# Performance work log

Measured on AMD Instinct MI355X. Metric: run time of the kernel, lower is better.

## Reference

```python
import jax, jax.numpy as jnp
import numpy as np

EMBED = 1024
HEADS = 16
HEAD_DIM = EMBED // HEADS


def setup_inputs() -> dict:
    key = jax.random.key(0)
    ks = jax.random.split(key, 10)
    s = 1.0 / np.sqrt(EMBED)
    inp = {
        "x": jax.random.normal(ks[0], (4, 2048, EMBED), dtype=jnp.float32),
        "mask": jax.random.randint(ks[1], (4, 2048), 0, 2, dtype=jnp.int32),
        "Wq": jax.random.uniform(ks[2], (EMBED, EMBED), jnp.float32, -s, s),
        "bq": jax.random.uniform(ks[3], (EMBED,), jnp.float32, -s, s),
        "Wk": jax.random.uniform(ks[4], (EMBED, EMBED), jnp.float32, -s, s),
        "bk": jax.random.uniform(ks[5], (EMBED,), jnp.float32, -s, s),
        "Wv": jax.random.uniform(ks[6], (EMBED, EMBED), jnp.float32, -s, s),
        "bv": jax.random.uniform(ks[7], (EMBED,), jnp.float32, -s, s),
        "Wo": jax.random.uniform(ks[8], (EMBED, EMBED), jnp.float32, -s, s),
        "bo": jax.random.uniform(ks[9], (EMBED,), jnp.float32, -s, s),
    }
    return inp


def reference(x, mask, Wq, bq, Wk, bk, Wv, bv, Wo, bo):
    B, S, E = x.shape
    scale = np.sqrt(HEAD_DIM).astype(np.float32)

    def split_heads(t):  # [B,S,E] -> [B,H,S,D]
        return t.reshape(B, S, HEADS, HEAD_DIM).transpose(0, 2, 1, 3)

    Q = split_heads(x @ Wq.T + bq)
    K = split_heads(x @ Wk.T + bk)
    V = split_heads(x @ Wv.T + bv)

    scores = jnp.einsum("bhqd,bhkd->bhqk", Q, K) / scale  # [B,H,S,S]
    # mask [B,S] broadcast over heads and query dim (key-padding mask)
    scores = jnp.where(mask[:, None, None, :] == 0, -jnp.inf, scores)
    weights = jax.nn.softmax(scores, axis=-1)
    out = jnp.einsum("bhqk,bhkd->bhqd", weights, V)  # [B,H,S,D]
    out = out.transpose(0, 2, 1, 3).reshape(B, S, E)
    return out @ Wo.T + bo
```

## Files before the change

kernel.cpp:

```cpp
#include <hip/hip_runtime.h>

#define BATCH 4
#define SEQ   2048
#define EMBED 1024
#define HEADS 16
#define HDIM  64
#define NTOK  (BATCH*SEQ)

typedef __attribute__((ext_vector_type(8)))  short short8;
typedef __attribute__((ext_vector_type(4)))  float f32x4;
typedef __attribute__((ext_vector_type(16))) float f32x16;

static __device__ __forceinline__ unsigned short f2bf(float f) {
    union { float f; unsigned u; } v; v.f = f;
    return (unsigned short)((v.u + 0x7FFFu + ((v.u >> 16) & 1u)) >> 16);
}
static __device__ __forceinline__ unsigned pk2bf(float lo, float hi) {
    union { float f; unsigned u; } a, b; a.f = lo; b.f = hi;
    return __builtin_amdgcn_perm(b.u + 0x8000u, a.u + 0x8000u, 0x07060302u);
}
static __device__ __forceinline__ void gload_lds16(const unsigned short* g, unsigned short* l) {
    __builtin_amdgcn_global_load_lds(
        (__attribute__((address_space(1))) void*)g,
        (__attribute__((address_space(3))) void*)l, 16, 0, 0);
}

__global__ void cast_f32_bf16(const float* __restrict__ in,
                              unsigned short* __restrict__ out, int n)
{
    int i = (blockIdx.x * 256 + threadIdx.x) * 8;
    if (i >= n) return;
    float4 a = *(const float4*)(in + i);
    float4 b = *(const float4*)(in + i + 4);
    union { int4 v; unsigned short u[8]; } pk;
    pk.u[0] = f2bf(a.x); pk.u[1] = f2bf(a.y); pk.u[2] = f2bf(a.z); pk.u[3] = f2bf(a.w);
    pk.u[4] = f2bf(b.x); pk.u[5] = f2bf(b.y); pk.u[6] = f2bf(b.z); pk.u[7] = f2bf(b.w);
    *(int4*)(out + i) = pk.v;
}

__global__ void cast4_f32_bf16(const float* __restrict__ a, const float* __restrict__ b,
                               const float* __restrict__ c, const float* __restrict__ d,
                               unsigned short* __restrict__ out)
{
    const float* srcs[4] = {a, b, c, d};
    const float* src = srcs[blockIdx.y];
    unsigned short* dst = out + (size_t)blockIdx.y * (EMBED * EMBED);
    int i = (blockIdx.x * 256 + threadIdx.x) * 8;
    float4 x = *(const float4*)(src + i);
    float4 y = *(const float4*)(src + i + 4);
    union { int4 v; unsigned short u[8]; } pk;
    pk.u[0] = f2bf(x.x); pk.u[1] = f2bf(x.y); pk.u[2] = f2bf(x.z); pk.u[3] = f2bf(x.w);
    pk.u[4] = f2bf(y.x); pk.u[5] = f2bf(y.y); pk.u[6] = f2bf(y.z); pk.u[7] = f2bf(y.w);
    *(int4*)(dst + i) = pk.v;
}

__device__ __forceinline__ void gemm_mainloop(const unsigned short* __restrict__ W,
                                              const unsigned short* __restrict__ X,
                                              int f0, int t0, f32x4 acc[4][4])
{
    __shared__ unsigned short Ws[128][32];
    __shared__ unsigned short Xs[128][32];

    const int tid  = threadIdx.x;
    const int lane = tid & 63, m = lane & 15, quad = lane >> 4;
    const int wid  = tid >> 6;
    const int wf   = (wid & 1) * 64;
    const int wt   = (wid >> 1) * 64;

    const int r    = tid >> 2, cc = tid & 3, sw = (tid >> 4) & 3;
    const int gcol = (cc ^ sw) << 3;
    const unsigned short* Wp = W + (size_t)(f0 + r) * EMBED + gcol;
    const unsigned short* Xp = X + (size_t)(t0 + r) * EMBED + gcol;
    unsigned short* WsL = &Ws[0][0] + tid * 8;
    unsigned short* XsL = &Xs[0][0] + tid * 8;

    const int qs = (quad ^ ((m >> 2) & 3)) << 3;

    for (int k0 = 0; k0 < EMBED; k0 += 32) {
        __syncthreads();
        gload_lds16(Wp + k0,              WsL);
        gload_lds16(Wp + k0 + 64 * EMBED, WsL + 2048);
        gload_lds16(Xp + k0,              XsL);
        gload_lds16(Xp + k0 + 64 * EMBED, XsL + 2048);
        __syncthreads();

        short8 af[4], bf4[4];
#pragma unroll
        for (int mb = 0; mb < 4; ++mb)
            af[mb] = *(const short8*)&Ws[wf + mb * 16 + m][qs];
#pragma unroll
        for (int nb = 0; nb < 4; ++nb)
            bf4[nb] = *(const short8*)&Xs[wt + nb * 16 + m][qs];
#pragma unroll
        for (int mb = 0; mb < 4; ++mb)
#pragma unroll
            for (int nb = 0; nb < 4; ++nb)
                acc[mb][nb] = __builtin_amdgcn_mfma_f32_16x16x32_bf16(
                    af[mb], bf4[nb], acc[mb][nb], 0, 0, 0);
    }
}

__global__ __launch_bounds__(256, 2)
void gemm_qkv(const unsigned short* __restrict__ Xb,
              const unsigned short* __restrict__ Wall,
              const float* __restrict__ bq, const float* __restrict__ bk,
              const float* __restrict__ bv,
              unsigned short* __restrict__ Qw, unsigned short* __restrict__ Kw,
              unsigned short* __restrict__ VtG)
{
    const int z  = blockIdx.z;
    const int f0 = blockIdx.x * 128, t0 = blockIdx.y * 128;
    f32x4 acc[4][4] = {};
    gemm_mainloop(Wall + (size_t)z * EMBED * EMBED, Xb, f0, t0, acc);

    const int lane = threadIdx.x & 63, m = lane & 15, quad = lane >> 4;
    const int wid  = threadIdx.x >> 6;
    const int wf = (wid & 1) * 64, wt = (wid >> 1) * 64;

    if (z < 2) {
        const float* bias = z ? bk : bq;
        unsigned short* C = z ? Kw : Qw;
#pragma unroll
        for (int mb = 0; mb < 4; ++mb) {
            const int feat = f0 + wf + mb * 16 + quad * 4;
            float4 bv4 = *(const float4*)&bias[feat];
#pragma unroll
            for (int nb = 0; nb < 4; ++nb) {
                const int tok = t0 + wt + nb * 16 + m;
                ushort4 pk;
                pk.x = f2bf(acc[mb][nb][0] + bv4.x);
                pk.y = f2bf(acc[mb][nb][1] + bv4.y);
                pk.z = f2bf(acc[mb][nb][2] + bv4.z);
                pk.w = f2bf(acc[mb][nb][3] + bv4.w);
                *(ushort4*)(C + (size_t)tok * EMBED + feat) = pk;
            }
        }
    } else {
        const int h = (f0 + wf) >> 6;
#pragma unroll
        for (int mb = 0; mb < 4; ++mb) {
            const int feat  = f0 + wf + mb * 16 + quad * 4;
            const int dbase = mb * 16 + quad * 4;
            float4 bv4 = *(const float4*)&bv[feat];
            float bb[4] = {bv4.x, bv4.y, bv4.z, bv4.w};
#pragma unroll
            for (int nb = 0; nb < 4; ++nb) {
                const int tok = t0 + wt + nb * 16 + m;
                const int b   = tok >> 11;
                const int s   = tok & (SEQ - 1);
#pragma unroll
                for (int r = 0; r < 4; ++r) {
                    VtG[((size_t)(b * HEADS + h) * HDIM + dbase + r) * SEQ + s] =
                        f2bf(acc[mb][nb][r] + bb[r]);
                }
            }
        }
    }
}

__global__ __launch_bounds__(256, 4)
void attn_mfma(const unsigned short* __restrict__ Qb,
               const unsigned short* __restrict__ Kb,
               const unsigned short* __restrict__ VtG,
               const int* __restrict__ mask,
               unsigned short* __restrict__ Ob)
{
    __shared__ unsigned short Ks[64][72];
    __shared__ unsigned short Vs[64][72];

    const int tid  = threadIdx.x;
    const int bid  = blockIdx.x;
    const int qb   = bid & 15;
    const int h    = (bid >> 4) & 15;
    const int b    = bid >> 8;
    const int wid  = tid >> 6, lane = tid & 63;
    const int q32  = lane & 31, hi = lane >> 5;
    const int tb   = b * SEQ;
    const int q    = qb * 128 + wid * 32 + q32;

    const unsigned short* qrow = Qb + (size_t)(tb + q) * EMBED + h * HDIM;
    short8 qf[4];
#pragma unroll
    for (int st = 0; st < 4; ++st)
        qf[st] = *(const short8*)(qrow + st * 16 + hi * 8);

    f32x16 o0, o1, z16;
#pragma unroll
    for (int i = 0; i < 16; ++i) { z16[i] = 0.f; }
    o0 = z16; o1 = z16;
    float lr = 0.f;

    const int sr = tid >> 2, sc = (tid & 3) * 16;
    const unsigned short* kSrc = Kb + (size_t)(tb + sr) * EMBED + h * HDIM + sc;
    const unsigned short* vSrc = VtG + ((size_t)(b * HEADS + h) * HDIM + sr) * SEQ + sc;

    const float SC = 0.180336880f;

    for (int kt = 0; kt < SEQ; kt += 64) {
        int4 kv0 = *(const int4*)(kSrc + (size_t)kt * EMBED);
        int4 kv1 = *(const int4*)(kSrc + (size_t)kt * EMBED + 8);
        int4 vv0 = *(const int4*)(vSrc + kt);
        int4 vv1 = *(const int4*)(vSrc + kt + 8);
        __syncthreads();
        *(int4*)&Ks[sr][sc]     = kv0;
        *(int4*)&Ks[sr][sc + 8] = kv1;
        *(int4*)&Vs[sr][sc]     = vv0;
        *(int4*)&Vs[sr][sc + 8] = vv1;
        __syncthreads();

#pragma unroll
        for (int kb = 0; kb < 2; ++kb) {
            float msk[16];
#pragma unroll
            for (int g = 0; g < 4; ++g) {
                int4 mv = *(const int4*)&mask[tb + kt + kb * 32 + g * 8 + hi * 4];
                msk[g * 4 + 0] = mv.x ? 1.f : 0.f;
                msk[g * 4 + 1] = mv.y ? 1.f : 0.f;
                msk[g * 4 + 2] = mv.z ? 1.f : 0.f;
                msk[g * 4 + 3] = mv.w ? 1.f : 0.f;
            }

            f32x16 s = z16;
#pragma unroll
            for (int st = 0; st < 4; ++st) {
                short8 kf = *(const short8*)&Ks[kb * 32 + q32][st * 16 + hi * 8];
                s = __builtin_amdgcn_mfma_f32_32x32x16_bf16(kf, qf[st], s, 0, 0, 0);
            }

            float p[16];
            float ps = 0.f;
#pragma unroll
            for (int i = 0; i < 16; ++i) {
                float e = msk[i] * __builtin_amdgcn_exp2f(s[i] * SC);
                p[i] = e; ps += e;
            }
            ps += __shfl_xor(ps, 32);
            lr += ps;

            unsigned D[8];
#pragma unroll
            for (int j = 0; j < 8; ++j) D[j] = pk2bf(p[2 * j], p[2 * j + 1]);

#pragma unroll
            for (int cl = 0; cl < 2; ++cl) {
                unsigned s0 = hi ? D[4 * cl + 0] : D[4 * cl + 2];
                unsigned s1 = hi ? D[4 * cl + 1] : D[4 * cl + 3];
                unsigned r0 = (unsigned)__shfl_xor((int)s0, 32);
                unsigned r1 = (unsigned)__shfl_xor((int)s1, 32);
                union { uint4 u; short8 s8; } fr;
                fr.u.x = hi ? r0 : D[4 * cl + 0];
                fr.u.y = hi ? r1 : D[4 * cl + 1];
                fr.u.z = hi ? D[4 * cl + 2] : r0;
                fr.u.w = hi ? D[4 * cl + 3] : r1;

                const int kcol = kb * 32 + cl * 16 + hi * 8;
                short8 vf0 = *(const short8*)&Vs[q32][kcol];
                short8 vf1 = *(const short8*)&Vs[32 + q32][kcol];
                o0 = __builtin_amdgcn_mfma_f32_32x32x16_bf16(vf0, fr.s8, o0, 0, 0, 0);
                o1 = __builtin_amdgcn_mfma_f32_32x32x16_bf16(vf1, fr.s8, o1, 0, 0, 0);
            }
        }
    }

    const float inv = 1.0f / lr;
    unsigned short* orow = Ob + (size_t)(tb + q) * EMBED + h * HDIM;
#pragma unroll
    for (int db = 0; db < 2; ++db) {
        const f32x16& oo = db ? o1 : o0;
#pragma unroll
        for (int qg = 0; qg < 4; ++qg) {
            ushort4 pk;
            pk.x = f2bf(oo[qg * 4 + 0] * inv);
            pk.y = f2bf(oo[qg * 4 + 1] * inv);
            pk.z = f2bf(oo[qg * 4 + 2] * inv);
            pk.w = f2bf(oo[qg * 4 + 3] * inv);
            *(ushort4*)(orow + db * 32 + qg * 8 + hi * 4) = pk;
        }
    }
}

__global__ __launch_bounds__(256, 2)
void gemm_o(const unsigned short* __restrict__ W, const unsigned short* __restrict__ X,
            const float* __restrict__ bias, float* __restrict__ Cout)
{
    const int f0 = blockIdx.x * 128, t0 = blockIdx.y * 128;
    f32x4 acc[4][4] = {};
    gemm_mainloop(W, X, f0, t0, acc);

    const int lane = threadIdx.x & 63, m = lane & 15, quad = lane >> 4;
    const int wid  = threadIdx.x >> 6;
    const int wf = (wid & 1) * 64, wt = (wid >> 1) * 64;
#pragma unroll
    for (int mb = 0; mb < 4; ++mb) {
        const int feat = f0 + wf + mb * 16 + quad * 4;
        float4 bv4 = *(const float4*)&bias[feat];
#pragma unroll
        for (int nb = 0; nb < 4; ++nb) {
            const int tok = t0 + wt + nb * 16 + m;
            float4 st;
            st.x = acc[mb][nb][0] + bv4.x;
            st.y = acc[mb][nb][1] + bv4.y;
            st.z = acc[mb][nb][2] + bv4.z;
            st.w = acc[mb][nb][3] + bv4.w;
            *(float4*)(Cout + (size_t)tok * EMBED + feat) = st;
        }
    }
}

extern "C" void kernel_launch(void* const* d_in, const int* in_sizes, int n_in,
                              void* d_out, int out_size, void* d_ws, size_t ws_size,
                              hipStream_t stream)
{
    const float* x    = (const float*)d_in[0];
    const int*   mask = (const int*)  d_in[1];
    const float* Wq   = (const float*)d_in[2];
    const float* bq   = (const float*)d_in[3];
    const float* Wk   = (const float*)d_in[4];
    const float* bk   = (const float*)d_in[5];
    const float* Wv   = (const float*)d_in[6];
    const float* bv   = (const float*)d_in[7];
    const float* Wo   = (const float*)d_in[8];
    const float* bo   = (const float*)d_in[9];
    float* out = (float*)d_out;

    const size_t NE = (size_t)NTOK * EMBED;
    const size_t WE = (size_t)EMBED * EMBED;
    unsigned short* Xb  = (unsigned short*)d_ws;
    unsigned short* Wqb = Xb + NE;
    unsigned short* Wob = Wqb + 3 * WE;
    unsigned short* Qw  = Wob + WE;
    unsigned short* Kw  = Qw + NE;
    unsigned short* VtG = Kw + NE;
    unsigned short* Ow  = Xb;

    cast_f32_bf16<<<NE / 2048, 256, 0, stream>>>(x, Xb, (int)NE);
    cast4_f32_bf16<<<dim3(WE / 2048, 4), 256, 0, stream>>>(Wq, Wk, Wv, Wo, Wqb);

    gemm_qkv<<<dim3(8, 64, 3), 256, 0, stream>>>(Xb, Wqb, bq, bk, bv, Qw, Kw, VtG);

    attn_mfma<<<BATCH * HEADS * (SEQ / 128), 256, 0, stream>>>(Qw, Kw, VtG, mask, Ow);

    gemm_o<<<dim3(8, 64), 256, 0, stream>>>(Wob, Ow, bo, out);
}
```

Measured before the change: 328.1 us.

## Fuse QKV GEMMs, fold mask and softmax scale into V/Q, compute rowsum via MFMA

Merges the two cast kernels into one launch. Fuses the three QKV projections into one kernel that shares the X tile across Wq/Wk/Wv and accumulates all three. The softmax scale is now folded into Q at projection time. The key mask is folded into V by zeroing masked tokens, and extra V rows carry the mask value so the softmax denominator comes out of an extra MFMA instead of a per-element mask multiply and a shuffle reduction. This removes mask loads and scalar work from the attention inner loop. The cost is a third accumulator tile in attention, more register pressure in the fused QKV kernel, a larger V buffer and an extra maskrow kernel.

```diff
diff --git a/kernel.cpp b/kernel.cpp
--- a/kernel.cpp
+++ b/kernel.cpp
@@ -6,6 +6,7 @@
 #define HEADS 16
 #define HDIM  64
 #define NTOK  (BATCH*SEQ)
+#define VROWS 72
 
 typedef __attribute__((ext_vector_type(8)))  short short8;
 typedef __attribute__((ext_vector_type(4)))  float f32x4;
@@ -25,43 +26,62 @@
         (__attribute__((address_space(3))) void*)l, 16, 0, 0);
 }
 
-__global__ void cast_f32_bf16(const float* __restrict__ in,
-                              unsigned short* __restrict__ out, int n)
-{
-    int i = (blockIdx.x * 256 + threadIdx.x) * 8;
-    if (i >= n) return;
-    float4 a = *(const float4*)(in + i);
-    float4 b = *(const float4*)(in + i + 4);
+#define SCQ 0.180336880f
+
+__global__ void cast_all(const float* __restrict__ x,
+                         const float* __restrict__ w0, const float* __restrict__ w1,
+                         const float* __restrict__ w2, const float* __restrict__ w3,
+                         unsigned short* __restrict__ xb,
+                         unsigned short* __restrict__ wb)
+{
+    const int bid = blockIdx.x;
+    const float* src;
+    unsigned short* dst;
+    int i;
+    if (bid < 4096) {
+        src = x; dst = xb; i = (bid * 256 + threadIdx.x) * 8;
+    } else {
+        const int wz = (bid - 4096) >> 9;
+        const float* ws[4] = {w0, w1, w2, w3};
+        src = ws[wz];
+        dst = wb + (size_t)wz * (EMBED * EMBED);
+        i = (((bid - 4096) & 511) * 256 + threadIdx.x) * 8;
+    }
+    float4 a = *(const float4*)(src + i);
+    float4 b = *(const float4*)(src + i + 4);
     union { int4 v; unsigned short u[8]; } pk;
     pk.u[0] = f2bf(a.x); pk.u[1] = f2bf(a.y); pk.u[2] = f2bf(a.z); pk.u[3] = f2bf(a.w);
     pk.u[4] = f2bf(b.x); pk.u[5] = f2bf(b.y); pk.u[6] = f2bf(b.z); pk.u[7] = f2bf(b.w);
-    *(int4*)(out + i) = pk.v;
-}
-
-__global__ void cast4_f32_bf16(const float* __restrict__ a, const float* __restrict__ b,
-                               const float* __restrict__ c, const float* __restrict__ d,
-                               unsigned short* __restrict__ out)
-{
-    const float* srcs[4] = {a, b, c, d};
-    const float* src = srcs[blockIdx.y];
-    unsigned short* dst = out + (size_t)blockIdx.y * (EMBED * EMBED);
-    int i = (blockIdx.x * 256 + threadIdx.x) * 8;
-    float4 x = *(const float4*)(src + i);
-    float4 y = *(const float4*)(src + i + 4);
-    union { int4 v; unsigned short u[8]; } pk;
-    pk.u[0] = f2bf(x.x); pk.u[1] = f2bf(x.y); pk.u[2] = f2bf(x.z); pk.u[3] = f2bf(x.w);
-    pk.u[4] = f2bf(y.x); pk.u[5] = f2bf(y.y); pk.u[6] = f2bf(y.z); pk.u[7] = f2bf(y.w);
     *(int4*)(dst + i) = pk.v;
 }
 
-__device__ __forceinline__ void gemm_mainloop(const unsigned short* __restrict__ W,
-                                              const unsigned short* __restrict__ X,
-                                              int f0, int t0, f32x4 acc[4][4])
-{
-    __shared__ unsigned short Ws[128][32];
+__global__ void maskrow(const int* __restrict__ mask, unsigned short* __restrict__ VtG)
+{
+    const int idx = blockIdx.x * 256 + threadIdx.x;
+    const int s  = idx & (SEQ - 1);
+    const int bh = idx >> 11;
+    const int b  = bh >> 4;
+    const unsigned short mv = mask[b * SEQ + s] ? (unsigned short)0x3F80 : (unsigned short)0;
+    const size_t base = (size_t)bh * VROWS * SEQ + s;
+#pragma unroll
+    for (int r = 64; r < 72; ++r)
+        VtG[base + (size_t)r * SEQ] = (r == 64 || r == 68) ? mv : (unsigned short)0;
+}
+
+__global__ __launch_bounds__(256, 2)
+void gemm_qkv(const unsigned short* __restrict__ Xb,
+              const unsigned short* __restrict__ Wall,
+              const float* __restrict__ bq, const float* __restrict__ bk,
+              const float* __restrict__ bv, const int* __restrict__ mask,
+              unsigned short* __restrict__ Qw, unsigned short* __restrict__ Kw,
+              unsigned short* __restrict__ VtG)
+{
+    __shared__ unsigned short Ws[3][128][32];
     __shared__ unsigned short Xs[128][32];
 
     const int tid  = threadIdx.x;
+    const int f0   = blockIdx.x * 128;
+    const int t0   = blockIdx.y * 128;
     const int lane = tid & 63, m = lane & 15, quad = lane >> 4;
     const int wid  = tid >> 6;
     const int wf   = (wid & 1) * 64;
@@ -69,90 +89,96 @@
 
     const int r    = tid >> 2, cc = tid & 3, sw = (tid >> 4) & 3;
     const int gcol = (cc ^ sw) << 3;
-    const unsigned short* Wp = W + (size_t)(f0 + r) * EMBED + gcol;
-    const unsigned short* Xp = X + (size_t)(t0 + r) * EMBED + gcol;
-    unsigned short* WsL = &Ws[0][0] + tid * 8;
+    const unsigned short* Xp = Xb + (size_t)(t0 + r) * EMBED + gcol;
+    const unsigned short* Wp = Wall + (size_t)(f0 + r) * EMBED + gcol;
     unsigned short* XsL = &Xs[0][0] + tid * 8;
+    unsigned short* WsL = &Ws[0][0][0] + tid * 8;
 
     const int qs = (quad ^ ((m >> 2) & 3)) << 3;
 
+    f32x4 aq[4][4] = {}, ak[4][4] = {}, av[4][4] = {};
+
     for (int k0 = 0; k0 < EMBED; k0 += 32) {
         __syncthreads();
-        gload_lds16(Wp + k0,              WsL);
-        gload_lds16(Wp + k0 + 64 * EMBED, WsL + 2048);
         gload_lds16(Xp + k0,              XsL);
         gload_lds16(Xp + k0 + 64 * EMBED, XsL + 2048);
-        __syncthreads();
-
-        short8 af[4], bf4[4];
-#pragma unroll
-        for (int mb = 0; mb < 4; ++mb)
-            af[mb] = *(const short8*)&Ws[wf + mb * 16 + m][qs];
+#pragma unroll
+        for (int z = 0; z < 3; ++z) {
+            const unsigned short* wz = Wp + (size_t)z * EMBED * EMBED + k0;
+            gload_lds16(wz,              WsL + z * 4096);
+            gload_lds16(wz + 64 * EMBED, WsL + z * 4096 + 2048);
+        }
+        __syncthreads();
+
+        short8 bf4[4];
 #pragma unroll
         for (int nb = 0; nb < 4; ++nb)
             bf4[nb] = *(const short8*)&Xs[wt + nb * 16 + m][qs];
-#pragma unroll
-        for (int mb = 0; mb < 4; ++mb)
-#pragma unroll
-            for (int nb = 0; nb < 4; ++nb)
-                acc[mb][nb] = __builtin_amdgcn_mfma_f32_16x16x32_bf16(
-                    af[mb], bf4[nb], acc[mb][nb], 0, 0, 0);
-    }
-}
-
-__global__ __launch_bounds__(256, 2)
-void gemm_qkv(const unsigned short* __restrict__ Xb,
-              const unsigned short* __restrict__ Wall,
-              const float* __restrict__ bq, const float* __restrict__ bk,
-              const float* __restrict__ bv,
-              unsigned short* __restrict__ Qw, unsigned short* __restrict__ Kw,
-              unsigned short* __restrict__ VtG)
-{
-    const int z  = blockIdx.z;
-    const int f0 = blockIdx.x * 128, t0 = blockIdx.y * 128;
-    f32x4 acc[4][4] = {};
-    gemm_mainloop(Wall + (size_t)z * EMBED * EMBED, Xb, f0, t0, acc);
-
-    const int lane = threadIdx.x & 63, m = lane & 15, quad = lane >> 4;
-    const int wid  = threadIdx.x >> 6;
-    const int wf = (wid & 1) * 64, wt = (wid >> 1) * 64;
-
-    if (z < 2) {
-        const float* bias = z ? bk : bq;
-        unsigned short* C = z ? Kw : Qw;
-#pragma unroll
-        for (int mb = 0; mb < 4; ++mb) {
-            const int feat = f0 + wf + mb * 16 + quad * 4;
-            float4 bv4 = *(const float4*)&bias[feat];
-#pragma unroll
-            for (int nb = 0; nb < 4; ++nb) {
-                const int tok = t0 + wt + nb * 16 + m;
-                ushort4 pk;
-                pk.x = f2bf(acc[mb][nb][0] + bv4.x);
-                pk.y = f2bf(acc[mb][nb][1] + bv4.y);
-                pk.z = f2bf(acc[mb][nb][2] + bv4.z);
-                pk.w = f2bf(acc[mb][nb][3] + bv4.w);
-                *(ushort4*)(C + (size_t)tok * EMBED + feat) = pk;
-            }
-        }
-    } else {
+
+#pragma unroll
+        for (int z = 0; z < 3; ++z) {
+            short8 af[4];
+#pragma unroll
+            for (int mb = 0; mb < 4; ++mb)
+                af[mb] = *(const short8*)&Ws[z][wf + mb * 16 + m][qs];
+            f32x4 (&acc)[4][4] = (z == 0) ? aq : (z == 1) ? ak : av;
+#pragma unroll
+            for (int mb = 0; mb < 4; ++mb)
+#pragma unroll
+                for (int nb = 0; nb < 4; ++nb)
+                    acc[mb][nb] = __builtin_amdgcn_mfma_f32_16x16x32_bf16(
+                        af[mb], bf4[nb], acc[mb][nb], 0, 0, 0);
+        }
+    }
+
+#pragma unroll
+    for (int mb = 0; mb < 4; ++mb) {
+        const int feat = f0 + wf + mb * 16 + quad * 4;
+        float4 bv4 = *(const float4*)&bq[feat];
+#pragma unroll
+        for (int nb = 0; nb < 4; ++nb) {
+            const int tok = t0 + wt + nb * 16 + m;
+            ushort4 pk;
+            pk.x = f2bf((aq[mb][nb][0] + bv4.x) * SCQ);
+            pk.y = f2bf((aq[mb][nb][1] + bv4.y) * SCQ);
+            pk.z = f2bf((aq[mb][nb][2] + bv4.z) * SCQ);
+            pk.w = f2bf((aq[mb][nb][3] + bv4.w) * SCQ);
+            *(ushort4*)(Qw + (size_t)tok * EMBED + feat) = pk;
+        }
+    }
+#pragma unroll
+    for (int mb = 0; mb < 4; ++mb) {
+        const int feat = f0 + wf + mb * 16 + quad * 4;
+        float4 bv4 = *(const float4*)&bk[feat];
+#pragma unroll
+        for (int nb = 0; nb < 4; ++nb) {
+            const int tok = t0 + wt + nb * 16 + m;
+            ushort4 pk;
+            pk.x = f2bf(ak[mb][nb][0] + bv4.x);
+            pk.y = f2bf(ak[mb][nb][1] + bv4.y);
+            pk.z = f2bf(ak[mb][nb][2] + bv4.z);
+            pk.w = f2bf(ak[mb][nb][3] + bv4.w);
+            *(ushort4*)(Kw + (size_t)tok * EMBED + feat) = pk;
+        }
+    }
+    {
         const int h = (f0 + wf) >> 6;
 #pragma unroll
-        for (int mb = 0; mb < 4; ++mb) {
-            const int feat  = f0 + wf + mb * 16 + quad * 4;
-            const int dbase = mb * 16 + quad * 4;
-            float4 bv4 = *(const float4*)&bv[feat];
-            float bb[4] = {bv4.x, bv4.y, bv4.z, bv4.w};
-#pragma unroll
-            for (int nb = 0; nb < 4; ++nb) {
-                const int tok = t0 + wt + nb * 16 + m;
-                const int b   = tok >> 11;
-                const int s   = tok & (SEQ - 1);
-#pragma unroll
-                for (int r = 0; r < 4; ++r) {
-                    VtG[((size_t)(b * HEADS + h) * HDIM + dbase + r) * SEQ + s] =
-                        f2bf(acc[mb][nb][r] + bb[r]);
-                }
+        for (int nb = 0; nb < 4; ++nb) {
+            const int tok = t0 + wt + nb * 16 + m;
+            const int b   = tok >> 11;
+            const int s   = tok & (SEQ - 1);
+            const float mf = mask[tok] ? 1.f : 0.f;
+            const size_t base = ((size_t)(b * HEADS + h) * VROWS) * SEQ + s;
+#pragma unroll
+            for (int mb = 0; mb < 4; ++mb) {
+                const int feat  = f0 + wf + mb * 16 + quad * 4;
+                const int dbase = mb * 16 + quad * 4;
+                float4 bv4 = *(const float4*)&bv[feat];
+                VtG[base + (size_t)(dbase + 0) * SEQ] = f2bf((av[mb][nb][0] + bv4.x) * mf);
+                VtG[base + (size_t)(dbase + 1) * SEQ] = f2bf((av[mb][nb][1] + bv4.y) * mf);
+                VtG[base + (size_t)(dbase + 2) * SEQ] = f2bf((av[mb][nb][2] + bv4.z) * mf);
+                VtG[base + (size_t)(dbase + 3) * SEQ] = f2bf((av[mb][nb][3] + bv4.w) * mf);
             }
         }
     }
@@ -162,11 +188,10 @@
 void attn_mfma(const unsigned short* __restrict__ Qb,
                const unsigned short* __restrict__ Kb,
                const unsigned short* __restrict__ VtG,
-               const int* __restrict__ mask,
                unsigned short* __restrict__ Ob)
 {
     __shared__ unsigned short Ks[64][72];
-    __shared__ unsigned short Vs[64][72];
+    __shared__ unsigned short Vs[96][72];
 
     const int tid  = threadIdx.x;
     const int bid  = blockIdx.x;
@@ -184,42 +209,42 @@
     for (int st = 0; st < 4; ++st)
         qf[st] = *(const short8*)(qrow + st * 16 + hi * 8);
 
-    f32x16 o0, o1, z16;
+    f32x16 o0, o1, o2, z16;
 #pragma unroll
     for (int i = 0; i < 16; ++i) { z16[i] = 0.f; }
-    o0 = z16; o1 = z16;
-    float lr = 0.f;
+    o0 = z16; o1 = z16; o2 = z16;
+
+    {
+        int* vz = (int*)&Vs[72][0];
+        for (int i = tid; i < 864; i += 256) vz[i] = 0;
+    }
 
     const int sr = tid >> 2, sc = (tid & 3) * 16;
     const unsigned short* kSrc = Kb + (size_t)(tb + sr) * EMBED + h * HDIM + sc;
-    const unsigned short* vSrc = VtG + ((size_t)(b * HEADS + h) * HDIM + sr) * SEQ + sc;
-
-    const float SC = 0.180336880f;
+    const size_t vhead = (size_t)(b * HEADS + h) * VROWS;
+    const unsigned short* vSrc = VtG + (vhead + sr) * SEQ + sc;
+    const unsigned short* vSrc2 = VtG + (vhead + 64 + (tid >> 2)) * SEQ + (tid & 3) * 16;
 
     for (int kt = 0; kt < SEQ; kt += 64) {
         int4 kv0 = *(const int4*)(kSrc + (size_t)kt * EMBED);
         int4 kv1 = *(const int4*)(kSrc + (size_t)kt * EMBED + 8);
         int4 vv0 = *(const int4*)(vSrc + kt);
         int4 vv1 = *(const int4*)(vSrc + kt + 8);
+        int4 mv0, mv1;
+        if (tid < 32) { mv0 = *(const int4*)(vSrc2 + kt); mv1 = *(const int4*)(vSrc2 + kt + 8); }
         __syncthreads();
         *(int4*)&Ks[sr][sc]     = kv0;
         *(int4*)&Ks[sr][sc + 8] = kv1;
         *(int4*)&Vs[sr][sc]     = vv0;
         *(int4*)&Vs[sr][sc + 8] = vv1;
+        if (tid < 32) {
+            *(int4*)&Vs[64 + (tid >> 2)][(tid & 3) * 16]     = mv0;
+            *(int4*)&Vs[64 + (tid >> 2)][(tid & 3) * 16 + 8] = mv1;
+        }
         __syncthreads();
 
 #pragma unroll
         for (int kb = 0; kb < 2; ++kb) {
-            float msk[16];
-#pragma unroll
-            for (int g = 0; g < 4; ++g) {
-                int4 mv = *(const int4*)&mask[tb + kt + kb * 32 + g * 8 + hi * 4];
-                msk[g * 4 + 0] = mv.x ? 1.f : 0.f;
-                msk[g * 4 + 1] = mv.y ? 1.f : 0.f;
-                msk[g * 4 + 2] = mv.z ? 1.f : 0.f;
-                msk[g * 4 + 3] = mv.w ? 1.f : 0.f;
-            }
-
             f32x16 s = z16;
 #pragma unroll
             for (int st = 0; st < 4; ++st) {
@@ -228,15 +253,8 @@
             }
 
             float p[16];
-            float ps = 0.f;
-#pragma unroll
-            for (int i = 0; i < 16; ++i) {
-                float e = msk[i] * __builtin_amdgcn_exp2f(s[i] * SC);
-                p[i] = e; ps += e;
-            }
-            ps += __shfl_xor(ps, 32);
-            lr += ps;
-
+#pragma unroll
+            for (int i = 0; i < 16; ++i) p[i] = __builtin_amdgcn_exp2f(s[i]);
             unsigned D[8];
 #pragma unroll
             for (int j = 0; j < 8; ++j) D[j] = pk2bf(p[2 * j], p[2 * j + 1]);
@@ -256,13 +274,15 @@
                 const int kcol = kb * 32 + cl * 16 + hi * 8;
                 short8 vf0 = *(const short8*)&Vs[q32][kcol];
                 short8 vf1 = *(const short8*)&Vs[32 + q32][kcol];
+                short8 vf2 = *(const short8*)&Vs[64 + q32][kcol];
                 o0 = __builtin_amdgcn_mfma_f32_32x32x16_bf16(vf0, fr.s8, o0, 0, 0, 0);
                 o1 = __builtin_amdgcn_mfma_f32_32x32x16_bf16(vf1, fr.s8, o1, 0, 0, 0);
+                o2 = __builtin_amdgcn_mfma_f32_32x32x16_bf16(vf2, fr.s8, o2, 0, 0, 0);
             }
         }
     }
 
-    const float inv = 1.0f / lr;
+    const float inv = 1.0f / o2[0];
     unsigned short* orow = Ob + (size_t)(tb + q) * EMBED + h * HDIM;
 #pragma unroll
     for (int db = 0; db < 2; ++db) {
@@ -283,13 +303,51 @@
 void gemm_o(const unsigned short* __restrict__ W, const unsigned short* __restrict__ X,
             const float* __restrict__ bias, float* __restrict__ Cout)
 {
-    const int f0 = blockIdx.x * 128, t0 = blockIdx.y * 128;
+    __shared__ unsigned short Ws[128][32];
+    __shared__ unsigned short Xs[128][32];
+
+    const int tid  = threadIdx.x;
+    const int f0   = blockIdx.x * 128;
+    const int t0   = blockIdx.y * 128;
+    const int lane = tid & 63, m = lane & 15, quad = lane >> 4;
+    const int wid  = tid >> 6;
+    const int wf   = (wid & 1) * 64;
+    const int wt   = (wid >> 1) * 64;
+
+    const int r    = tid >> 2, cc = tid & 3, sw = (tid >> 4) & 3;
+    const int gcol = (cc ^ sw) << 3;
+    const unsigned short* Wp = W + (size_t)(f0 + r) * EMBED + gcol;
+    const unsigned short* Xp = X + (size_t)(t0 + r) * EMBED + gcol;
+    unsigned short* WsL = &Ws[0][0] + tid * 8;
+    unsigned short* XsL = &Xs[0][0] + tid * 8;
+
+    const int qs = (quad ^ ((m >> 2) & 3)) << 3;
+
     f32x4 acc[4][4] = {};
-    gemm_mainloop(W, X, f0, t0, acc);
-
-    const int lane = threadIdx.x & 63, m = lane & 15, quad = lane >> 4;
-    const int wid  = threadIdx.x >> 6;
-    const int wf = (wid & 1) * 64, wt = (wid >> 1) * 64;
+
+    for (int k0 = 0; k0 < EMBED; k0 += 32) {
+        __syncthreads();
+        gload_lds16(Wp + k0,              WsL);
+        gload_lds16(Wp + k0 + 64 * EMBED, WsL + 2048);
+        gload_lds16(Xp + k0,              XsL);
+        gload_lds16(Xp + k0 + 64 * EMBED, XsL + 2048);
+        __syncthreads();
+
+        short8 af[4], bf4[4];
+#pragma unroll
+        for (int mb = 0; mb < 4; ++mb)
+            af[mb] = *(const short8*)&Ws[wf + mb * 16 + m][qs];
+#pragma unroll
+        for (int nb = 0; nb < 4; ++nb)
+            bf4[nb] = *(const short8*)&Xs[wt + nb * 16 + m][qs];
+#pragma unroll
+        for (int mb = 0; mb < 4; ++mb)
+#pragma unroll
+            for (int nb = 0; nb < 4; ++nb)
+                acc[mb][nb] = __builtin_amdgcn_mfma_f32_16x16x32_bf16(
+                    af[mb], bf4[nb], acc[mb][nb], 0, 0, 0);
+    }
+
 #pragma unroll
     for (int mb = 0; mb < 4; ++mb) {
         const int feat = f0 + wf + mb * 16 + quad * 4;
@@ -325,6 +383,7 @@
 
     const size_t NE = (size_t)NTOK * EMBED;
     const size_t WE = (size_t)EMBED * EMBED;
+    const size_t VE = (size_t)BATCH * HEADS * VROWS * SEQ;
     unsigned short* Xb  = (unsigned short*)d_ws;
     unsigned short* Wqb = Xb + NE;
     unsigned short* Wob = Wqb + 3 * WE;
@@ -333,12 +392,13 @@
     unsigned short* VtG = Kw + NE;
     unsigned short* Ow  = Xb;
 
-    cast_f32_bf16<<<NE / 2048, 256, 0, stream>>>(x, Xb, (int)NE);
-    cast4_f32_bf16<<<dim3(WE / 2048, 4), 256, 0, stream>>>(Wq, Wk, Wv, Wo, Wqb);
-
-    gemm_qkv<<<dim3(8, 64, 3), 256, 0, stream>>>(Xb, Wqb, bq, bk, bv, Qw, Kw, VtG);
-
-    attn_mfma<<<BATCH * HEADS * (SEQ / 128), 256, 0, stream>>>(Qw, Kw, VtG, mask, Ow);
+    cast_all<<<4096 + 2048, 256, 0, stream>>>(x, Wq, Wk, Wv, Wo, Xb, Wqb);
+
+    maskrow<<<(BATCH * HEADS * SEQ) / 256, 256, 0, stream>>>(mask, VtG);
+
+    gemm_qkv<<<dim3(8, 64), 256, 0, stream>>>(Xb, Wqb, bq, bk, bv, mask, Qw, Kw, VtG);
+
+    attn_mfma<<<BATCH * HEADS * (SEQ / 128), 256, 0, stream>>>(Qw, Kw, VtG, Ow);
 
     gemm_o<<<dim3(8, 64), 256, 0, stream>>>(Wob, Ow, bo, out);
 }
```

New measurement: 289.6 us. 11.7% less time.
